# Performance work log

Measured on AMD Instinct MI355X. Metric: run time of the kernel, lower is better.

Reference implementation:

```python
import jax, jax.numpy as jnp
import numpy as np

WINDOWS = [1, 3, 5]
LN_EPS = 1e-5
N, C, H, W = 16, 64, 160, 160


def conv1x1(x, w, b):
    # x: [N,C,H,W], w: [O,C], b: [O]  (1x1 conv == channel matmul)
    return jnp.einsum('nchw,oc->nohw', x, w) + b[None, :, None, None]


def _patch_idx(H_, W_, kh, kw, sh, sw):
    nh = (H_ - kh) // sh + 1
    nw = (W_ - kw) // sw + 1
    hi = jnp.arange(nh)[:, None] * sh + jnp.arange(kh)[None, :]  # [nh,kh]
    wi = jnp.arange(nw)[:, None] * sw + jnp.arange(kw)[None, :]  # [nw,kw]
    return nh, nw, hi, wi


def unfold(x, kh, kw, sh, sw):
    # matches torch.nn.functional.unfold: out [N, C*kh*kw, nh*nw]
    n, c, H_, W_ = x.shape
    nh, nw, hi, wi = _patch_idx(H_, W_, kh, kw, sh, sw)
    p = x[:, :, hi[:, None, :, None], wi[None, :, None, :]]      # [N,C,nh,nw,kh,kw]
    p = jnp.transpose(p, (0, 1, 4, 5, 2, 3))                      # [N,C,kh,kw,nh,nw]
    return p.reshape(n, c * kh * kw, nh * nw)


def fold(u, H_, W_, kh, kw, sh, sw):
    # matches torch.nn.functional.fold (overlap add)
    n = u.shape[0]
    nh, nw, hi, wi = _patch_idx(H_, W_, kh, kw, sh, sw)
    c = u.shape[1] // (kh * kw)
    p = u.reshape(n, c, kh, kw, nh, nw)
    p = jnp.transpose(p, (0, 1, 4, 5, 2, 3))                      # [N,C,nh,nw,kh,kw]
    out = jnp.zeros((n, c, H_, W_), u.dtype)
    return out.at[:, :, hi[:, None, :, None], wi[None, :, None, :]].add(p)


def psa(x, ch_wv_w, ch_wv_b, ch_wq_w, ch_wq_b, ch_wz_w, ch_wz_b,
        ln_g, ln_b, sp_wv_w, sp_wv_b, sp_wq_w, sp_wq_b):
    # Polarized Self-Attention (parallel): channel-only + spatial-only branches
    b, c, h, w = x.shape
    hw = h * w
    c2 = c // 2
    # channel-only branch
    wv = conv1x1(x, ch_wv_w, ch_wv_b).reshape(b, c2, hw)
    wq = jax.nn.softmax(conv1x1(x, ch_wq_w, ch_wq_b).reshape(b, hw), axis=-1)
    wz = jnp.einsum('bch,bh->bc', wv, wq)                         # [b,c2]
    z = jnp.einsum('bc,oc->bo', wz, ch_wz_w) + ch_wz_b            # [b,c]
    mu = jnp.mean(z, axis=-1, keepdims=True)
    var = jnp.var(z, axis=-1, keepdims=True)
    zn = (z - mu) * jax.lax.rsqrt(var + LN_EPS) * ln_g + ln_b     # LayerNorm(c)
    ch_out = jax.nn.sigmoid(zn)[:, :, None, None] * x
    # spatial-only branch
    swv = conv1x1(x, sp_wv_w, sp_wv_b).reshape(b, c2, hw)
    swq = jax.nn.softmax(jnp.mean(conv1x1(x, sp_wq_w, sp_wq_b), axis=(2, 3)), axis=-1)
    smap = jax.nn.sigmoid(jnp.einsum('bc,bch->bh', swq, swv)).reshape(b, 1, h, w)
    return ch_out + smap * x


def setup_inputs() -> dict:
    key = jax.random.key(0)
    ks = jax.random.split(key, 12)
    c, c2, nw_ = C, C // 2, len(WINDOWS)
    s = 0.05
    return {
        'x': jax.random.normal(ks[0], (N, C, H, W), jnp.float32),
        'exp_w': jax.random.normal(ks[1], (nw_ * c, c), jnp.float32) * s,
        'exp_b': jnp.zeros((nw_ * c,), jnp.float32),
        'res_w': jax.random.normal(ks[2], (c, nw_ * c), jnp.float32) * s,
        'res_b': jnp.zeros((c,), jnp.float32),
        'fus_w': jax.random.normal(ks[3], (c, c), jnp.float32) * s,
        'fus_b': jnp.zeros((c,), jnp.float32),
        'ch_wv_w': jax.random.normal(ks[4], (c2, c), jnp.float32) * s,
        'ch_wv_b': jnp.zeros((c2,), jnp.float32),
        'ch_wq_w': jax.random.normal(ks[5], (1, c), jnp.float32) * s,
        'ch_wq_b': jnp.zeros((1,), jnp.float32),
        'ch_wz_w': jax.random.normal(ks[6], (c, c2), jnp.float32) * s,
        'ch_wz_b': jnp.zeros((c,), jnp.float32),
        'ln_g': jnp.ones((c,), jnp.float32),
        'ln_b': jnp.zeros((c,), jnp.float32),
        'sp_wv_w': jax.random.normal(ks[7], (c2, c), jnp.float32) * s,
        'sp_wv_b': jnp.zeros((c2,), jnp.float32),
        'sp_wq_w': jax.random.normal(ks[8], (c2, c), jnp.float32) * s,
        'sp_wq_b': jnp.zeros((c2,), jnp.float32),
    }


def reference(x, exp_w, exp_b, res_w, res_b, fus_w, fus_b,
              ch_wv_w, ch_wv_b, ch_wq_w, ch_wq_b, ch_wz_w, ch_wz_b,
              ln_g, ln_b, sp_wv_w, sp_wv_b, sp_wq_w, sp_wq_b):
    n, c, h, w = x.shape
    psa_params = (ch_wv_w, ch_wv_b, ch_wq_w, ch_wq_b, ch_wz_w, ch_wz_b,
                  ln_g, ln_b, sp_wv_w, sp_wv_b, sp_wq_w, sp_wq_b)
    ex = conv1x1(x, exp_w, exp_b)                                 # [N, 3C, H, W]
    chunks = jnp.split(ex, len(WINDOWS), axis=1)
    outs = []
    for i, win in enumerate(WINDOWS):
        sh, sw = h // win, w // win
        kh, kw = sh + h % win, sw + w % win
        u = unfold(chunks[i], kh, kw, sh, sw)
        # faithful to torch source: raw view (no permute) into patch images
        a = psa(u.reshape(-1, c, kh, kw), *psa_params)
        a = a.reshape(n, c * kh * kw, win * win)
        cnt = fold(jnp.ones_like(a), h, w, kh, kw, sh, sw)        # overlap counts
        outs.append(fold(a, h, w, kh, kw, sh, sw) / cnt)
    cat = jnp.concatenate(outs, axis=1) + ex
    return conv1x1(conv1x1(cat, res_w, res_b) + x, fus_w, fus_b)
```

## Files before the change

kernel.cpp:

```cpp
#include <hip/hip_runtime.h>
#include <hip/hip_bf16.h>

typedef __hip_bfloat16 bf16;
typedef __attribute__((ext_vector_type(4))) unsigned int u32x4;
typedef __attribute__((ext_vector_type(4))) float f32x4;
typedef __attribute__((ext_vector_type(8))) short bf16x8;
#define DEV __device__ __forceinline__


constexpr int FO_Q     = 0;
constexpr int FO_SMAP  = 1239104;
constexpr int FO_XM    = 2478208;
constexpr int FO_T     = 2514048;
constexpr int FO_SIGA  = 2549888;
constexpr int FO_G     = 2585728;
constexpr int FO_BM    = 2621568;
constexpr int FO_BINV  = 2622128;
constexpr int FO_GB    = 2622688;
constexpr int FO_EXPT  = 2623248;
constexpr int FO_EXPB  = 2635536;
constexpr int FO_WBIGT = 2635728;
constexpr int FO_BCOMB = 2652112;
constexpr int FO_WFRAG = 2652176;
constexpr int FB_SIZE  = 2660368;

__device__ unsigned short g_ex_u[78643200];
__device__ float          g_fb[FB_SIZE];

template<int WIN> struct WP;
template<> struct WP<1> { static constexpr int WI=0, SH=160, KH=160, K=25600, P=1,  B=16,  QOFF=0,      BOFF=0;   };
template<> struct WP<3> { static constexpr int WI=1, SH=53,  KH=54,  K=2916,  P=9,  B=144, QOFF=409600, BOFF=16;  };
template<> struct WP<5> { static constexpr int WI=2, SH=32,  KH=32,  K=1024,  P=25, B=400, QOFF=829504, BOFF=160; };

template<int WIN> DEV void decomp(int f, int& c, int& kidx, int& p) {
  constexpr int P = WP<WIN>::P, K = WP<WIN>::K;
  int m;
  if constexpr (P == 1) { p = 0; m = f; }
  else { m = f / P; p = f - m * P; }
  c = m / K; kidx = m - c * K;
}

template<int WIN> DEV void stepK(int& c, int& kidx, int& p) {
  constexpr int K = WP<WIN>::K, P = WP<WIN>::P;
  if constexpr (P == 1) { kidx += K; }
  else {
    constexpr int KMP = K % P, KDP = K / P;
    if constexpr (KMP == 0) { kidx += KDP; }
    else { p += KMP; if (p >= P) { p -= P; kidx += KDP + 1; } else kidx += KDP; }
  }
  if (kidx >= K) { kidx -= K; ++c; }
}

template<int WIN> DEV int pix(int kidx, int p) {
  constexpr int KH = WP<WIN>::KH, SH = WP<WIN>::SH;
  if constexpr (WIN == 1) return kidx;
  int ki = kidx / KH, kj = kidx - ki * KH;
  int ph = p / WIN,  pw = p - ph * WIN;
  return (ph * SH + ki) * 160 + pw * SH + kj;
}

DEV unsigned short bfbits(float f) {
  bf16 b = __float2bfloat16(f);
  unsigned short u;
  __builtin_memcpy(&u, &b, 2);
  return u;
}

DEV void store8bf(bf16* p, const unsigned short* ob) {
  u32x4 v = { (unsigned)ob[0] | ((unsigned)ob[1] << 16),
              (unsigned)ob[2] | ((unsigned)ob[3] << 16),
              (unsigned)ob[4] | ((unsigned)ob[5] << 16),
              (unsigned)ob[6] | ((unsigned)ob[7] << 16) };
  *(u32x4*)p = v;
}

DEV bf16x8 as_bf16x8(u32x4 v) {
  union { u32x4 u; bf16x8 b; } x; x.u = v; return x.b;
}

DEV void wave_reduce64_atomic(float* dst, float (&part)[64], int lane) {
#pragma unroll
  for (int s = 0; s < 6; ++s) {
    const int m = 1 << s, half = 32 >> s;
#pragma unroll
    for (int i = 0; i < half; ++i) {
      float lo = part[i], hi = part[i + half];
      float keep = (lane & m) ? hi : lo;
      float sv   = (lane & m) ? lo : hi;
      float recv = __shfl_xor(sv, m, 64);
      part[i] = keep + recv;
    }
  }
  int chn = (int)(__brev((unsigned)lane) >> 26);
  atomicAdd(dst + chn, part[0]);
}

__global__ __launch_bounds__(256)
void k_prep(const float* __restrict__ exp_w, const float* __restrict__ exp_b,
            const float* __restrict__ res_w, const float* __restrict__ res_b,
            const float* __restrict__ fus_w, const float* __restrict__ fus_b) {
  float* fb = g_fb;
  int gt = blockIdx.x * 256 + threadIdx.x;
  if (gt < 12288) {
    int oc = gt % 192, f = gt / 192;
    float a = 0.f;
    for (int o = 0; o < 64; ++o)
      a += fus_w[f*64+o] * res_w[o*192+oc];
    fb[FO_WBIGT + oc*64 + f] = a;
  } else if (gt < 16384) {
    int t2 = gt - 12288; int o = t2 % 64, f = t2 / 64;
    fb[FO_WBIGT + (192+o)*64 + f] = fus_w[f*64+o];
  } else if (gt < 16448) {
    int f = gt - 16384;
    float a = fus_b[f];
    for (int o = 0; o < 64; ++o)
      a += fus_w[f*64+o] * res_b[o];
    fb[FO_BCOMB + f] = a;
  } else if (gt < 28736) {
    int t3 = gt - 16448; int o = t3 % 192, c = t3 / 192;
    fb[FO_EXPT + c*192 + o] = exp_w[o*64+c];
  } else if (gt < 28928) {
    int o = gt - 28736;
    fb[FO_EXPB + o] = exp_b[o];
  } else if (gt < 28928 + 71680) {
    fb[FO_XM + gt - 28928] = 0.f;
  }
}

__global__ __launch_bounds__(256)
void k_prep2() {
  float* fb = g_fb;
  bf16* wf = (bf16*)(fb + FO_WFRAG);
  int t = blockIdx.x * 256 + threadIdx.x;
  int j  = t & 7;
  int l  = (t >> 3) & 63;
  int ks = (t >> 9) & 7;
  int wv = t >> 12;
  int k = ks*32 + (l >> 4)*8 + j;
  int o = wv*16 + (l & 15);
  wf[t] = __float2bfloat16(fb[FO_WBIGT + k*64 + o]);
}

__global__ __launch_bounds__(256)
void k_ex(const float* __restrict__ x) {
  const float* fb = g_fb;
  bf16* ex = (bf16*)g_ex_u;
  __shared__ float xs[64*64];
  int blk = blockIdx.x; int n = blk / 400; int s0 = (blk % 400) * 64;
  int tid = threadIdx.x;
  for (int e = tid; e < 4096; e += 256) {
    int c = e >> 6, px = e & 63;
    xs[e] = x[(n*64 + c)*25600 + s0 + px];
  }
  __syncthreads();
  int px = tid & 63;
  int o0 = __builtin_amdgcn_readfirstlane((tid >> 6) * 48);
  float acc[48];
#pragma unroll
  for (int j = 0; j < 48; ++j) acc[j] = fb[FO_EXPB + o0 + j];
  const float* wT = fb + FO_EXPT;
  for (int c = 0; c < 64; ++c) {
    float xv = xs[(c << 6) + px];
    const float* wr = wT + c*192 + o0;
#pragma unroll
    for (int j = 0; j < 48; ++j) acc[j] += wr[j] * xv;
  }
  bf16* eo = ex + (size_t)(n*192 + o0)*25600 + s0 + px;
#pragma unroll
  for (int j = 0; j < 48; ++j) eo[(size_t)j*25600] = __float2bfloat16(acc[j]);
}

template<int WIN, int CH, int CHUNK, int ITERS>
DEV void p1_body(int idx, const float* __restrict__ chq_w, float wqb) {
  using W = WP<WIN>;
  constexpr int K = W::K, P = W::P, CK = 64*K, WI = W::WI, QOFF = W::QOFF,
                BOFF = W::BOFF;
  float* fb = g_fb;
  const bf16* ex = (const bf16*)g_ex_u;
  int bi = idx / CH, ch = idx - bi*CH;
  int n = bi / P, bl = bi - n*P; int bg = BOFF + bi;
  int base = ch*CHUNK;
  int send = (base + CHUNK < K) ? base + CHUNK : K;
  const bf16* exn = ex + (size_t)(n*192 + WI*64)*25600;
  float* qout = fb + FO_Q + QOFF + (size_t)bi*K;
  int tid = threadIdx.x, lane = tid & 63;
  float wq[64];
#pragma unroll
  for (int j = 0; j < 64; ++j) wq[j] = chq_w[j];
  float part[64];
#pragma unroll
  for (int j = 0; j < 64; ++j) part[j] = 0.f;
  for (int it = 0; it < ITERS; ++it) {
    int sp = base + it*256 + tid;
    if (sp < send) {
      int f = bl*CK + sp;
      int c, kidx, p; decomp<WIN>(f, c, kidx, p);
      float dot = 0.f;
#pragma unroll
      for (int j = 0; j < 64; ++j) {
        float v = __bfloat162float(exn[c*25600 + pix<WIN>(kidx, p)]);
        part[j] += v;
        dot += wq[j] * v;
        stepK<WIN>(c, kidx, p);
      }
      qout[sp] = dot + wqb;
    }
  }
  wave_reduce64_atomic(fb + FO_XM + bg*64, part, lane);
}

__global__ __launch_bounds__(256, 2)
void k_p1all(const float* __restrict__ chq_w, const float* __restrict__ chq_b) {
  float wqb = chq_b[0];
  int blk = blockIdx.x;
  if (blk < 400)      p1_body<1,25,1024,4>(blk,       chq_w, wqb);
  else if (blk < 832) p1_body<3, 3, 972,4>(blk - 400, chq_w, wqb);
  else                p1_body<5, 2, 512,2>(blk - 832, chq_w, wqb);
}

__global__ __launch_bounds__(256)
void k_bstats(const float* __restrict__ spq_w, const float* __restrict__ spq_b,
              const float* __restrict__ spv_w, const float* __restrict__ spv_b) {
  float* fb = g_fb;
  __shared__ float red[256]; __shared__ float sqs[32]; __shared__ float swq[32];
  int bg = blockIdx.x, tid = threadIdx.x;
  int Kk, qo, bi;
  if (bg < 16)       { Kk = 25600; qo = 0;      bi = bg;       }
  else if (bg < 160) { Kk = 2916;  qo = 409600; bi = bg - 16;  }
  else               { Kk = 1024;  qo = 829504; bi = bg - 160; }
  const float* lg = fb + FO_Q + qo + (size_t)bi*Kk;
  float m = -1e30f;
  for (int s = tid; s < Kk; s += 256) m = fmaxf(m, lg[s]);
  red[tid] = m; __syncthreads();
  for (int st = 128; st; st >>= 1) { if (tid < st) red[tid] = fmaxf(red[tid], red[tid+st]); __syncthreads(); }
  float M = red[0]; __syncthreads();
  float ss = 0.f;
  for (int s = tid; s < Kk; s += 256) ss += __expf(lg[s] - M);
  red[tid] = ss; __syncthreads();
  for (int st = 128; st; st >>= 1) { if (tid < st) red[tid] += red[tid+st]; __syncthreads(); }
  if (tid == 0) { fb[FO_BM + bg] = M; fb[FO_BINV + bg] = 1.f / red[0]; }
  const float* xm_b = fb + FO_XM + bg*64;
  float rK = 1.f / (float)Kk;
  if (tid < 32) {
    float a = spq_b[tid];
    for (int c = 0; c < 64; ++c)
      a += spq_w[tid*64 + c] * (xm_b[c] * rK);
    sqs[tid] = a;
  }
  __syncthreads();
  if (tid == 0) {
    float mx = -1e30f;
    for (int o = 0; o < 32; ++o) mx = fmaxf(mx, sqs[o]);
    float z = 0.f;
    for (int o = 0; o < 32; ++o) { float e = __expf(sqs[o] - mx); swq[o] = e; z += e; }
    float rz = 1.f / z;
    for (int o = 0; o < 32; ++o) swq[o] *= rz;
  }
  __syncthreads();
  if (tid < 64) {
    float a = 0.f;
    for (int o = 0; o < 32; ++o) a += swq[o] * spv_w[o*64 + tid];
    fb[FO_G + bg*64 + tid] = a;
  }
  if (tid == 64) {
    float gb = 0.f;
    for (int o = 0; o < 32; ++o) gb += swq[o] * spv_b[o];
    fb[FO_GB + bg] = gb;
  }
}

template<int WIN, int CH, int CHUNK, int ITERS>
DEV void p2_body(int idx) {
  using W = WP<WIN>;
  constexpr int K = W::K, P = W::P, CK = 64*K, WI = W::WI, QOFF = W::QOFF,
                BOFF = W::BOFF;
  float* fb = g_fb;
  const bf16* ex = (const bf16*)g_ex_u;
  int bi = idx / CH, ch = idx - bi*CH;
  int n = bi / P, bl = bi - n*P; int bg = BOFF + bi;
  int base = ch*CHUNK;
  int send = (base + CHUNK < K) ? base + CHUNK : K;
  const bf16* exn = ex + (size_t)(n*192 + WI*64)*25600;
  const float* qin = fb + FO_Q + QOFF + (size_t)bi*K;
  float* so = fb + FO_SMAP + QOFF + (size_t)bi*K;
  float M = fb[FO_BM + bg], inv = fb[FO_BINV + bg];
  float gbs = fb[FO_GB + bg];
  int tid = threadIdx.x, lane = tid & 63;
  float gs[64];
#pragma unroll
  for (int j = 0; j < 64; ++j) gs[j] = fb[FO_G + bg*64 + j];
  float part[64];
#pragma unroll
  for (int j = 0; j < 64; ++j) part[j] = 0.f;
  for (int it = 0; it < ITERS; ++it) {
    int sp = base + it*256 + tid;
    if (sp < send) {
      float qv = __expf(qin[sp] - M) * inv;
      int f = bl*CK + sp;
      int c, kidx, p; decomp<WIN>(f, c, kidx, p);
      float dot = 0.f;
#pragma unroll
      for (int j = 0; j < 64; ++j) {
        float v = __bfloat162float(exn[c*25600 + pix<WIN>(kidx, p)]);
        part[j] += qv * v;
        dot += gs[j] * v;
        stepK<WIN>(c, kidx, p);
      }
      so[sp] = 1.f / (1.f + __expf(-(dot + gbs)));
    }
  }
  wave_reduce64_atomic(fb + FO_T + bg*64, part, lane);
}

__global__ __launch_bounds__(256, 2)
void k_p2all() {
  int blk = blockIdx.x;
  if (blk < 400)      p2_body<1,25,1024,4>(blk);
  else if (blk < 832) p2_body<3, 3, 972,4>(blk - 400);
  else                p2_body<5, 2, 512,2>(blk - 832);
}

__global__ __launch_bounds__(64)
void k_zln(const float* __restrict__ chv_w, const float* __restrict__ chv_b,
           const float* __restrict__ chz_w, const float* __restrict__ chz_b,
           const float* __restrict__ ln_g,  const float* __restrict__ ln_b) {
  float* fb = g_fb;
  __shared__ float wzs[32]; __shared__ float zsh[64]; __shared__ float mom[2];
  int bg = blockIdx.x, tid = threadIdx.x;
  const float* t_b = fb + FO_T + bg*64;
  if (tid < 32) {
    float a = chv_b[tid];
    for (int c = 0; c < 64; ++c)
      a += chv_w[tid*64 + c] * t_b[c];
    wzs[tid] = a;
  }
  __syncthreads();
  float zv = chz_b[tid];
  for (int o = 0; o < 32; ++o)
    zv += chz_w[tid*32 + o] * wzs[o];
  zsh[tid] = zv;
  __syncthreads();
  if (tid == 0) {
    float mu = 0.f;
    for (int j = 0; j < 64; ++j) mu += zsh[j];
    mu *= (1.f/64.f);
    float m2 = 0.f;
    for (int j = 0; j < 64; ++j) { float d = zsh[j] - mu; m2 += d*d; }
    m2 *= (1.f/64.f);
    mom[0] = mu; mom[1] = rsqrtf(m2 + 1e-5f);
  }
  __syncthreads();
  float zn = (zv - mom[0]) * mom[1] * ln_g[tid] + ln_b[tid];
  fb[FO_SIGA + bg*64 + tid] = 1.f / (1.f + __expf(-zn));
}

template<int WIN> DEV void gate_rows2(int n, int h, int w, int px,
                                      const bf16* __restrict__ ex,
                                      const float* __restrict__ fb,
                                      bf16* extT) {
  using W = WP<WIN>;
  constexpr int SH = W::SH, KH = W::KH, K = W::K, P = W::P, WI = W::WI,
                QOFF = W::QOFF, BOFF = W::BOFF;
  int s = h*160 + w;
  const bf16* exr = ex + (size_t)(n*192 + WI*64)*25600 + s;
  const float* smap = fb + FO_SMAP + QOFF + (size_t)(n*P)*K;
  const float* sg   = fb + FO_SIGA + (size_t)(BOFF + n*P)*64;
  int swz = (px & 7) << 3;
  unsigned short ob[8];
  if constexpr (WIN == 1) {
    float sm = smap[s];
    for (int c0 = 0; c0 < 64; c0 += 8) {
#pragma unroll
      for (int cc = 0; cc < 8; ++cc) {
        int c = c0 + cc;
        float exv = __bfloat162float(exr[(size_t)c*25600]);
        ob[cc] = bfbits(exv * (1.f + sg[c] + sm));
      }
      store8bf(&extT[px*256 + ((WI*64 + c0) ^ swz)], ob);
    }
  } else {
    int phmin = (h >= KH) ? (h - KH)/SH + 1 : 0;
    int phmax = (WIN-1 < h/SH) ? WIN-1 : h/SH;
    int pwmin = (w >= KH) ? (w - KH)/SH + 1 : 0;
    int pwmax = (WIN-1 < w/SH) ? WIN-1 : w/SH;
    int cf[4]; int s0s[4]; int np = 0;
    for (int ph = phmin; ph <= phmax; ++ph)
      for (int pw = pwmin; pw <= pwmax; ++pw) {
        int ki = h - ph*SH, kj = w - pw*SH;
        unsigned base0 = (unsigned)((ki*KH + kj)*P + ph*WIN + pw);
        unsigned q = base0 / (unsigned)K;
        cf[np] = (int)q; s0s[np] = (int)(base0 - q*(unsigned)K); ++np;
      }
    float rc = 1.f / (float)np;
    int hi[4]; float smv[4];
#pragma unroll
    for (int t = 0; t < 4; ++t)
      if (t < np) { hi[t] = cf[t] >> 6; smv[t] = smap[hi[t]*K + s0s[t]]; }
    for (int c0 = 0; c0 < 64; c0 += 8) {
#pragma unroll
      for (int cc = 0; cc < 8; ++cc) {
        float gsum = 0.f;
#pragma unroll
        for (int t = 0; t < 4; ++t) {
          if (t < np) {
            int v = cf[t];
            int h2 = v >> 6;
            if (h2 != hi[t]) { hi[t] = h2; smv[t] = smap[h2*K + s0s[t]]; }
            gsum += sg[v] + smv[t];
            cf[t] = v + P;
          }
        }
        int c = c0 + cc;
        float exv = __bfloat162float(exr[(size_t)c*25600]);
        ob[cc] = bfbits(exv * (1.f + gsum * rc));
      }
      store8bf(&extT[px*256 + ((WI*64 + c0) ^ swz)], ob);
    }
  }
}

__global__ __launch_bounds__(256)
void k_final(const float* __restrict__ x, float* __restrict__ out) {
  const float* fb = g_fb;
  const bf16* ex = (const bf16*)g_ex_u;
  __shared__ __align__(16) bf16 extT[64*256];
  int blk = blockIdx.x; int n = blk / 400; int s0 = (blk % 400) * 64;
  int tid = threadIdx.x;
  int rg = tid >> 6; int px = tid & 63;
  int s = s0 + px; int h = s / 160; int w = s - h*160;
  if (rg == 3) {
    int swz = (px & 7) << 3;
    unsigned short ob[8];
    for (int c0 = 0; c0 < 64; c0 += 8) {
#pragma unroll
      for (int cc = 0; cc < 8; ++cc)
        ob[cc] = bfbits(x[(size_t)(n*64 + c0 + cc)*25600 + s]);
      store8bf(&extT[px*256 + ((192 + c0) ^ swz)], ob);
    }
  } else if (rg == 0) gate_rows2<1>(n, h, w, px, ex, fb, extT);
  else if (rg == 1)   gate_rows2<3>(n, h, w, px, ex, fb, extT);
  else                gate_rows2<5>(n, h, w, px, ex, fb, extT);
  __syncthreads();

  int wv = tid >> 6; int l = tid & 63;
  int lx = l & 15, g = l >> 4;
  const u32x4* wfA = (const u32x4*)(fb + FO_WFRAG);
  u32x4 af[8];
#pragma unroll
  for (int ks = 0; ks < 8; ++ks) af[ks] = wfA[(wv*8 + ks)*64 + l];
  f32x4 acc[4];
#pragma unroll
  for (int pt = 0; pt < 4; ++pt) acc[pt] = f32x4{0.f, 0.f, 0.f, 0.f};
#pragma unroll
  for (int ks = 0; ks < 8; ++ks) {
#pragma unroll
    for (int pt = 0; pt < 4; ++pt) {
      int pxx = pt*16 + lx;
      const u32x4* bp = (const u32x4*)&extT[pxx*256 + ((ks*32 + g*8) ^ ((pxx & 7) << 3))];
      acc[pt] = __builtin_amdgcn_mfma_f32_16x16x32_bf16(
                  as_bf16x8(af[ks]), as_bf16x8(*bp), acc[pt], 0, 0, 0);
    }
  }
  float bia[4];
#pragma unroll
  for (int r = 0; r < 4; ++r) bia[r] = fb[FO_BCOMB + wv*16 + g*4 + r];
#pragma unroll
  for (int pt = 0; pt < 4; ++pt) {
#pragma unroll
    for (int r = 0; r < 4; ++r)
      out[(size_t)(n*64 + wv*16 + g*4 + r)*25600 + s0 + pt*16 + lx] = acc[pt][r] + bia[r];
  }
}

extern "C" void kernel_launch(void* const* d_in, const int* in_sizes, int n_in,
                              void* d_out, int out_size, void* d_ws, size_t ws_size,
                              hipStream_t stream) {
  const float* x     = (const float*)d_in[0];
  const float* exp_w = (const float*)d_in[1];
  const float* exp_b = (const float*)d_in[2];
  const float* res_w = (const float*)d_in[3];
  const float* res_b = (const float*)d_in[4];
  const float* fus_w = (const float*)d_in[5];
  const float* fus_b = (const float*)d_in[6];
  const float* chv_w = (const float*)d_in[7];
  const float* chv_b = (const float*)d_in[8];
  const float* chq_w = (const float*)d_in[9];
  const float* chq_b = (const float*)d_in[10];
  const float* chz_w = (const float*)d_in[11];
  const float* chz_b = (const float*)d_in[12];
  const float* ln_g  = (const float*)d_in[13];
  const float* ln_b  = (const float*)d_in[14];
  const float* spv_w = (const float*)d_in[15];
  const float* spv_b = (const float*)d_in[16];
  const float* spq_w = (const float*)d_in[17];
  const float* spq_b = (const float*)d_in[18];
  float* out = (float*)d_out;

  k_prep<<<393, 256, 0, stream>>>(exp_w, exp_b, res_w, res_b, fus_w, fus_b);
  k_prep2<<<64, 256, 0, stream>>>();
  k_ex<<<6400, 256, 0, stream>>>(x);

  k_p1all<<<1632, 256, 0, stream>>>(chq_w, chq_b);

  k_bstats<<<560, 256, 0, stream>>>(spq_w, spq_b, spv_w, spv_b);

  k_p2all<<<1632, 256, 0, stream>>>();

  k_zln<<<560, 64, 0, stream>>>(chv_w, chv_b, chz_w, chz_b, ln_g, ln_b);

  k_final<<<6400, 256, 0, stream>>>(x, out);
}
```

Measured before the change: 838.4 us.

## Add pixel-major bf16 copy of expanded features and x for vectorized reads

k_ex now also writes a second pixel-major buffer holding the 192 expanded channels plus a bf16 copy of x, 256 bf16 per pixel, alongside the existing channel-planar buffer. The window-1 paths of the p1/p2 passes and all gating in k_final read this layout with 16-byte vector loads instead of 64 strided scalar loads. The goal is better coalescing and fewer load instructions in the bandwidth-bound passes. In exchange, k_ex does an extra ~200MB of writes, its thread split changes from 4x48 channels to 3x64 plus one x-transpose group, and more global memory is used.

```diff
diff --git a/kernel.cpp b/kernel.cpp
--- a/kernel.cpp
+++ b/kernel.cpp
@@ -25,6 +25,7 @@
 constexpr int FB_SIZE  = 2660368;
 
 __device__ unsigned short g_ex_u[78643200];
+__device__ unsigned short g_ex2_u[104857600];
 __device__ float          g_fb[FB_SIZE];
 
 template<int WIN> struct WP;
@@ -64,6 +65,12 @@
   unsigned short u;
   __builtin_memcpy(&u, &b, 2);
   return u;
+}
+
+DEV float bf2f(unsigned short u) {
+  bf16 b;
+  __builtin_memcpy(&b, &u, 2);
+  return __bfloat162float(b);
 }
 
 DEV void store8bf(bf16* p, const unsigned short* ob) {
@@ -144,7 +151,8 @@
 __global__ __launch_bounds__(256)
 void k_ex(const float* __restrict__ x) {
   const float* fb = g_fb;
-  bf16* ex = (bf16*)g_ex_u;
+  bf16* ex  = (bf16*)g_ex_u;
+  bf16* ex2 = (bf16*)g_ex2_u;
   __shared__ float xs[64*64];
   int blk = blockIdx.x; int n = blk / 400; int s0 = (blk % 400) * 64;
   int tid = threadIdx.x;
@@ -154,20 +162,40 @@
   }
   __syncthreads();
   int px = tid & 63;
-  int o0 = __builtin_amdgcn_readfirstlane((tid >> 6) * 48);
-  float acc[48];
-#pragma unroll
-  for (int j = 0; j < 48; ++j) acc[j] = fb[FO_EXPB + o0 + j];
+  int rg = tid >> 6;
+  bf16* e2row = ex2 + (size_t)(n*25600 + s0 + px)*256;
+  unsigned short ob[8];
+  if (rg == 3) {
+#pragma unroll
+    for (int r = 0; r < 8; ++r) {
+#pragma unroll
+      for (int i = 0; i < 8; ++i)
+        ob[i] = bfbits(xs[(r*8 + i)*64 + px]);
+      store8bf(e2row + 192 + r*8, ob);
+    }
+    return;
+  }
+  int o0 = __builtin_amdgcn_readfirstlane(rg * 64);
+  float acc[64];
+#pragma unroll
+  for (int j = 0; j < 64; ++j) acc[j] = fb[FO_EXPB + o0 + j];
   const float* wT = fb + FO_EXPT;
   for (int c = 0; c < 64; ++c) {
     float xv = xs[(c << 6) + px];
     const float* wr = wT + c*192 + o0;
 #pragma unroll
-    for (int j = 0; j < 48; ++j) acc[j] += wr[j] * xv;
+    for (int j = 0; j < 64; ++j) acc[j] += wr[j] * xv;
   }
   bf16* eo = ex + (size_t)(n*192 + o0)*25600 + s0 + px;
 #pragma unroll
-  for (int j = 0; j < 48; ++j) eo[(size_t)j*25600] = __float2bfloat16(acc[j]);
+  for (int j = 0; j < 64; ++j) eo[(size_t)j*25600] = __float2bfloat16(acc[j]);
+#pragma unroll
+  for (int r = 0; r < 8; ++r) {
+#pragma unroll
+    for (int i = 0; i < 8; ++i)
+      ob[i] = bfbits(acc[r*8 + i]);
+    store8bf(e2row + o0 + r*8, ob);
+  }
 }
 
 template<int WIN, int CH, int CHUNK, int ITERS>
@@ -176,7 +204,8 @@
   constexpr int K = W::K, P = W::P, CK = 64*K, WI = W::WI, QOFF = W::QOFF,
                 BOFF = W::BOFF;
   float* fb = g_fb;
-  const bf16* ex = (const bf16*)g_ex_u;
+  const bf16* ex  = (const bf16*)g_ex_u;
+  const bf16* ex2 = (const bf16*)g_ex2_u;
   int bi = idx / CH, ch = idx - bi*CH;
   int n = bi / P, bl = bi - n*P; int bg = BOFF + bi;
   int base = ch*CHUNK;
@@ -193,15 +222,31 @@
   for (int it = 0; it < ITERS; ++it) {
     int sp = base + it*256 + tid;
     if (sp < send) {
-      int f = bl*CK + sp;
-      int c, kidx, p; decomp<WIN>(f, c, kidx, p);
       float dot = 0.f;
-#pragma unroll
-      for (int j = 0; j < 64; ++j) {
-        float v = __bfloat162float(exn[c*25600 + pix<WIN>(kidx, p)]);
-        part[j] += v;
-        dot += wq[j] * v;
-        stepK<WIN>(c, kidx, p);
+      if constexpr (WIN == 1) {
+        const u32x4* e2 = (const u32x4*)(ex2 + (size_t)(n*25600 + sp)*256);
+#pragma unroll
+        for (int r = 0; r < 8; ++r) {
+          u32x4 v = e2[r];
+#pragma unroll
+          for (int i = 0; i < 4; ++i) {
+            int c = r*8 + 2*i;
+            float lo = bf2f((unsigned short)(v[i] & 0xffffu));
+            float hi = bf2f((unsigned short)(v[i] >> 16));
+            part[c]   += lo;  dot += wq[c]   * lo;
+            part[c+1] += hi;  dot += wq[c+1] * hi;
+          }
+        }
+      } else {
+        int f = bl*CK + sp;
+        int c, kidx, p; decomp<WIN>(f, c, kidx, p);
+#pragma unroll
+        for (int j = 0; j < 64; ++j) {
+          float v = __bfloat162float(exn[c*25600 + pix<WIN>(kidx, p)]);
+          part[j] += v;
+          dot += wq[j] * v;
+          stepK<WIN>(c, kidx, p);
+        }
       }
       qout[sp] = dot + wqb;
     }
@@ -275,7 +320,8 @@
   constexpr int K = W::K, P = W::P, CK = 64*K, WI = W::WI, QOFF = W::QOFF,
                 BOFF = W::BOFF;
   float* fb = g_fb;
-  const bf16* ex = (const bf16*)g_ex_u;
+  const bf16* ex  = (const bf16*)g_ex_u;
+  const bf16* ex2 = (const bf16*)g_ex2_u;
   int bi = idx / CH, ch = idx - bi*CH;
   int n = bi / P, bl = bi - n*P; int bg = BOFF + bi;
   int base = ch*CHUNK;
@@ -296,15 +342,31 @@
     int sp = base + it*256 + tid;
     if (sp < send) {
       float qv = __expf(qin[sp] - M) * inv;
-      int f = bl*CK + sp;
-      int c, kidx, p; decomp<WIN>(f, c, kidx, p);
       float dot = 0.f;
-#pragma unroll
-      for (int j = 0; j < 64; ++j) {
-        float v = __bfloat162float(exn[c*25600 + pix<WIN>(kidx, p)]);
-        part[j] += qv * v;
-        dot += gs[j] * v;
-        stepK<WIN>(c, kidx, p);
+      if constexpr (WIN == 1) {
+        const u32x4* e2 = (const u32x4*)(ex2 + (size_t)(n*25600 + sp)*256);
+#pragma unroll
+        for (int r = 0; r < 8; ++r) {
+          u32x4 v = e2[r];
+#pragma unroll
+          for (int i = 0; i < 4; ++i) {
+            int c = r*8 + 2*i;
+            float lo = bf2f((unsigned short)(v[i] & 0xffffu));
+            float hi = bf2f((unsigned short)(v[i] >> 16));
+            part[c]   += qv * lo;  dot += gs[c]   * lo;
+            part[c+1] += qv * hi;  dot += gs[c+1] * hi;
+          }
+        }
+      } else {
+        int f = bl*CK + sp;
+        int c, kidx, p; decomp<WIN>(f, c, kidx, p);
+#pragma unroll
+        for (int j = 0; j < 64; ++j) {
+          float v = __bfloat162float(exn[c*25600 + pix<WIN>(kidx, p)]);
+          part[j] += qv * v;
+          dot += gs[j] * v;
+          stepK<WIN>(c, kidx, p);
+        }
       }
       so[sp] = 1.f / (1.f + __expf(-(dot + gbs)));
     }
@@ -354,29 +416,34 @@
   fb[FO_SIGA + bg*64 + tid] = 1.f / (1.f + __expf(-zn));
 }
 
-template<int WIN> DEV void gate_rows2(int n, int h, int w, int px,
-                                      const bf16* __restrict__ ex,
+template<int WIN> DEV void gate_rows3(int n, int s, int h, int w, int px,
                                       const float* __restrict__ fb,
+                                      const bf16* __restrict__ e2row,
                                       bf16* extT) {
   using W = WP<WIN>;
   constexpr int SH = W::SH, KH = W::KH, K = W::K, P = W::P, WI = W::WI,
                 QOFF = W::QOFF, BOFF = W::BOFF;
-  int s = h*160 + w;
-  const bf16* exr = ex + (size_t)(n*192 + WI*64)*25600 + s;
   const float* smap = fb + FO_SMAP + QOFF + (size_t)(n*P)*K;
   const float* sg   = fb + FO_SIGA + (size_t)(BOFF + n*P)*64;
+  const u32x4* src = (const u32x4*)(e2row + WI*64);
+  u32x4 vv[8];
+#pragma unroll
+  for (int r = 0; r < 8; ++r) vv[r] = src[r];
   int swz = (px & 7) << 3;
   unsigned short ob[8];
   if constexpr (WIN == 1) {
     float sm = smap[s];
-    for (int c0 = 0; c0 < 64; c0 += 8) {
-#pragma unroll
-      for (int cc = 0; cc < 8; ++cc) {
-        int c = c0 + cc;
-        float exv = __bfloat162float(exr[(size_t)c*25600]);
-        ob[cc] = bfbits(exv * (1.f + sg[c] + sm));
+#pragma unroll
+    for (int r = 0; r < 8; ++r) {
+#pragma unroll
+      for (int i = 0; i < 4; ++i) {
+        int c = r*8 + 2*i;
+        float lo = bf2f((unsigned short)(vv[r][i] & 0xffffu));
+        float hi = bf2f((unsigned short)(vv[r][i] >> 16));
+        ob[2*i]   = bfbits(lo * (1.f + sg[c]   + sm));
+        ob[2*i+1] = bfbits(hi * (1.f + sg[c+1] + sm));
       }
-      store8bf(&extT[px*256 + ((WI*64 + c0) ^ swz)], ob);
+      store8bf(&extT[px*256 + ((WI*64 + r*8) ^ swz)], ob);
     }
   } else {
     int phmin = (h >= KH) ? (h - KH)/SH + 1 : 0;
@@ -392,11 +459,12 @@
         cf[np] = (int)q; s0s[np] = (int)(base0 - q*(unsigned)K); ++np;
       }
     float rc = 1.f / (float)np;
-    int hi[4]; float smv[4];
+    int hi4[4]; float smv[4];
 #pragma unroll
     for (int t = 0; t < 4; ++t)
-      if (t < np) { hi[t] = cf[t] >> 6; smv[t] = smap[hi[t]*K + s0s[t]]; }
-    for (int c0 = 0; c0 < 64; c0 += 8) {
+      if (t < np) { hi4[t] = cf[t] >> 6; smv[t] = smap[hi4[t]*K + s0s[t]]; }
+#pragma unroll
+    for (int r = 0; r < 8; ++r) {
 #pragma unroll
       for (int cc = 0; cc < 8; ++cc) {
         float gsum = 0.f;
@@ -405,41 +473,40 @@
           if (t < np) {
             int v = cf[t];
             int h2 = v >> 6;
-            if (h2 != hi[t]) { hi[t] = h2; smv[t] = smap[h2*K + s0s[t]]; }
+            if (h2 != hi4[t]) { hi4[t] = h2; smv[t] = smap[h2*K + s0s[t]]; }
             gsum += sg[v] + smv[t];
             cf[t] = v + P;
           }
         }
-        int c = c0 + cc;
-        float exv = __bfloat162float(exr[(size_t)c*25600]);
-        ob[cc] = bfbits(exv * (1.f + gsum * rc));
+        unsigned wd = vv[r][cc >> 1];
+        unsigned short eb = (cc & 1) ? (unsigned short)(wd >> 16)
+                                     : (unsigned short)(wd & 0xffffu);
+        ob[cc] = bfbits(bf2f(eb) * (1.f + gsum * rc));
       }
-      store8bf(&extT[px*256 + ((WI*64 + c0) ^ swz)], ob);
+      store8bf(&extT[px*256 + ((WI*64 + r*8) ^ swz)], ob);
     }
   }
 }
 
 __global__ __launch_bounds__(256)
-void k_final(const float* __restrict__ x, float* __restrict__ out) {
+void k_final(float* __restrict__ out) {
   const float* fb = g_fb;
-  const bf16* ex = (const bf16*)g_ex_u;
+  const bf16* ex2 = (const bf16*)g_ex2_u;
   __shared__ __align__(16) bf16 extT[64*256];
   int blk = blockIdx.x; int n = blk / 400; int s0 = (blk % 400) * 64;
   int tid = threadIdx.x;
   int rg = tid >> 6; int px = tid & 63;
   int s = s0 + px; int h = s / 160; int w = s - h*160;
+  const bf16* e2row = ex2 + (size_t)(n*25600 + s)*256;
   if (rg == 3) {
+    const u32x4* src = (const u32x4*)(e2row + 192);
     int swz = (px & 7) << 3;
-    unsigned short ob[8];
-    for (int c0 = 0; c0 < 64; c0 += 8) {
-#pragma unroll
-      for (int cc = 0; cc < 8; ++cc)
-        ob[cc] = bfbits(x[(size_t)(n*64 + c0 + cc)*25600 + s]);
-      store8bf(&extT[px*256 + ((192 + c0) ^ swz)], ob);
-    }
-  } else if (rg == 0) gate_rows2<1>(n, h, w, px, ex, fb, extT);
-  else if (rg == 1)   gate_rows2<3>(n, h, w, px, ex, fb, extT);
-  else                gate_rows2<5>(n, h, w, px, ex, fb, extT);
+#pragma unroll
+    for (int r = 0; r < 8; ++r)
+      *(u32x4*)&extT[px*256 + ((192 + r*8) ^ swz)] = src[r];
+  } else if (rg == 0) gate_rows3<1>(n, s, h, w, px, fb, e2row, extT);
+  else if (rg == 1)   gate_rows3<3>(n, s, h, w, px, fb, e2row, extT);
+  else                gate_rows3<5>(n, s, h, w, px, fb, e2row, extT);
   __syncthreads();
 
   int wv = tid >> 6; int l = tid & 63;
@@ -508,5 +575,5 @@
 
   k_zln<<<560, 64, 0, stream>>>(chv_w, chv_b, chz_w, chz_b, ln_g, ln_b);
 
-  k_final<<<6400, 256, 0, stream>>>(x, out);
-}
+  k_final<<<6400, 256, 0, stream>>>(out);
+}
```

Result: slower. 859.5 us (+2.5%).
